# Performance work log

Hardware: AMD Instinct MI355X
Metric: run time of the kernel (lower is better)

## Reference

```python
import jax, jax.numpy as jnp
import numpy as np

HEADS = 6
FILTERS = (16, 32, 64)
V_FEATS = 11
N_NODES = 30000
N_EDGES = 480000


def setup_inputs() -> dict:
    key = jax.random.key(0)
    ks = jax.random.split(key, 20)
    d = {}
    d["x_int"] = jax.random.normal(ks[0], (N_NODES, V_FEATS), jnp.float32)
    d["x_nh"] = jax.random.normal(ks[1], (N_NODES, V_FEATS), jnp.float32)
    d["ei_int"] = jax.random.randint(ks[2], (2, N_EDGES), 0, N_NODES, jnp.int32)
    d["ei_nh"] = jax.random.randint(ks[3], (2, N_EDGES), 0, N_NODES, jnp.int32)
    f_in = V_FEATS
    kidx = 4
    for i, f in enumerate(FILTERS, 1):
        s = 1.0 / np.sqrt(f_in)
        d[f"W{i}"] = (jax.random.normal(ks[kidx], (f_in, HEADS * f), jnp.float32) * s); kidx += 1
        sa = 1.0 / np.sqrt(f)
        d[f"a{i}s"] = (jax.random.normal(ks[kidx], (HEADS, f), jnp.float32) * sa); kidx += 1
        d[f"a{i}d"] = (jax.random.normal(ks[kidx], (HEADS, f), jnp.float32) * sa); kidx += 1
        f_in = HEADS * f
    d["Wd"] = jax.random.normal(ks[kidx], (2 * HEADS * FILTERS[-1], 1), jnp.float32) * 0.05
    d["bd"] = jnp.zeros((1,), jnp.float32)
    return d


def _gat_layer(h, src, dst, W, a_s, a_d):
    """One multi-head graph-attention (DGAT) layer, heads concatenated.
    h: [N, F_in]; W: [F_in, H*F_out]; a_s, a_d: [H, F_out]."""
    N = h.shape[0]
    H, Fo = a_s.shape
    z = (h @ W).reshape(N, H, Fo)                      # [N, H, Fo]
    e_src = jnp.einsum('nhf,hf->nh', z, a_s)           # [N, H]
    e_dst = jnp.einsum('nhf,hf->nh', z, a_d)
    e = jax.nn.leaky_relu(e_src[src] + e_dst[dst], 0.2)  # [E, H]
    # softmax over incoming edges of each destination node
    e_max = jax.ops.segment_max(e, dst, num_segments=N)  # [N, H] (-inf for empty)
    ex = jnp.exp(e - e_max[dst])
    denom = jax.ops.segment_sum(ex, dst, num_segments=N)
    alpha = ex / (denom[dst] + 1e-16)                   # [E, H]
    msg = z[src] * alpha[:, :, None]                    # [E, H, Fo]
    out = jax.ops.segment_sum(msg, dst, num_segments=N) # [N, H, Fo]
    return jax.nn.elu(out).reshape(N, H * Fo)


def reference(x_int, x_nh, W1, a1s, a1d, W2, a2s, a2d, W3, a3s, a3d, Wd, bd, ei_int, ei_nh):
    layers = [(W1, a1s, a1d), (W2, a2s, a2d), (W3, a3s, a3d)]

    def run(h, ei):
        src, dst = ei[0], ei[1]
        for (W, a_s, a_d) in layers:
            h = _gat_layer(h, src, dst, W, a_s, a_d)
        return h

    hi = run(x_int, ei_int)   # [N, 384]
    hn = run(x_nh, ei_nh)     # [N, 384]
    x = jnp.concatenate([hi, hn], axis=1)       # [N, 768]
    x = jnp.sum(x, axis=0).reshape(1, -1)       # [1, 768] sum pooling
    norm = jnp.maximum(jnp.linalg.norm(x, axis=1, keepdims=True), 1e-12)
    x = x / norm                                # F.normalize
    x = x @ Wd + bd                             # Dense, linear nonlin
    return jnp.squeeze(x, 1)                    # [1]
```

## Files before the change

kernel.cpp:

```cpp
#include <hip/hip_runtime.h>
#include <math.h>

#define N_NODES 30000
#define N_EDGES 480000
#define HEADS   6
#define NN2 (2 * N_NODES)
#define NE2 (2 * N_EDGES)

typedef __attribute__((ext_vector_type(8))) short bf16x8;
typedef __attribute__((ext_vector_type(4))) float f32x4;
typedef __attribute__((ext_vector_type(2))) float f32x2;

__device__ __forceinline__ unsigned short f2bf(float f) {
    unsigned u = __float_as_uint(f);
    u += 0x7fffu + ((u >> 16) & 1u);
    return (unsigned short)(u >> 16);
}

__global__ void gemm1_es_kernel(const float* __restrict__ x0, const float* __restrict__ x1,
                                const float* __restrict__ W, const float* __restrict__ a_s,
                                const float* __restrict__ a_d,
                                unsigned char* __restrict__ zf8b, float* __restrict__ es8,
                                float* __restrict__ ed8) {
    constexpr int K = 11, HF = 96, TM = 16, Fo = 16;
    __shared__ float hs[TM * K];
    const int m0 = blockIdx.x * TM;
    const float* h = (m0 < N_NODES) ? (x0 + (size_t)m0 * K)
                                    : (x1 + (size_t)(m0 - N_NODES) * K);
    const int j = blockIdx.y * 64 + threadIdx.x;
    for (int idx = threadIdx.x; idx < TM * K; idx += 64) hs[idx] = h[idx];
    __syncthreads();
    if (j >= HF) return;
    float acc[TM];
#pragma unroll
    for (int m = 0; m < TM; ++m) acc[m] = 0.f;
    for (int k = 0; k < K; ++k) {
        float w = W[k * HF + j];
#pragma unroll
        for (int m = 0; m < TM; ++m) acc[m] = fmaf(hs[m * K + k], w, acc[m]);
    }
    const float as_v = a_s[j];
    const float ad_v = a_d[j];
    const int hh = j >> 4;
    const int fo = j & 15;
#pragma unroll
    for (int m = 0; m < TM; ++m) {
        const int pk = __builtin_amdgcn_cvt_pk_fp8_f32(acc[m], acc[m], 0, false);
        zf8b[((size_t)hh * NN2 + (m0 + m)) * Fo + fo] = (unsigned char)pk;
    }
#pragma unroll
    for (int m = 0; m < TM; ++m) {
        float ep = acc[m] * as_v;
        float dp = acc[m] * ad_v;
#pragma unroll
        for (int d = 1; d < 16; d <<= 1) {
            ep += __shfl_xor(ep, d);
            dp += __shfl_xor(dp, d);
        }
        if ((threadIdx.x & 15) == 0) {
            es8[(size_t)(m0 + m) * 8 + hh] = ep;
            ed8[(size_t)(m0 + m) * 8 + hh] = dp;
        }
    }
}

__global__ void convert_wt_kernel(const float* __restrict__ W, unsigned short* __restrict__ Wt,
                                  int K, int HF) {
    const int idx = blockIdx.x * 256 + threadIdx.x;
    if (idx >= K * HF) return;
    const int k = idx / HF;
    const int n = idx - k * HF;
    Wt[n * K + k] = f2bf(W[idx]);
}

template <int K, int HF>
__global__ __launch_bounds__(256) void gemm_es_kernel(
        const unsigned short* __restrict__ hbf, const unsigned short* __restrict__ Wt,
        const float* __restrict__ a_s, const float* __restrict__ a_d,
        unsigned char* __restrict__ zf8b, float* __restrict__ es8,
        float* __restrict__ ed8) {
    constexpr int KSTEPS = K / 32;
    constexpr int Fo  = HF / HEADS;
    constexpr int TPH = Fo / 16;
    const int wid = blockIdx.x * 4 + (threadIdx.x >> 6);
    if (wid >= NN2 / 16) return;
    const int lane = threadIdx.x & 63;
    const int r16  = lane & 15;
    const int quad = lane >> 4;
    const int m0 = wid * 16;

    bf16x8 afrag[KSTEPS];
    const unsigned short* ap = hbf + (size_t)(m0 + r16) * K + quad * 8;
#pragma unroll
    for (int i = 0; i < KSTEPS; ++i) afrag[i] = *(const bf16x8*)(ap + i * 32);

    const unsigned short* bp = Wt + (size_t)r16 * K + quad * 8;
    float es_p[4] = {0.f, 0.f, 0.f, 0.f};
    float ed_p[4] = {0.f, 0.f, 0.f, 0.f};
    for (int t = 0; t < HF / 16; ++t) {
        f32x4 acc = {0.f, 0.f, 0.f, 0.f};
        const unsigned short* bpt = bp + (size_t)t * 16 * K;
#pragma unroll
        for (int i = 0; i < KSTEPS; ++i) {
            const bf16x8 bfrag = *(const bf16x8*)(bpt + i * 32);
            acc = __builtin_amdgcn_mfma_f32_16x16x32_bf16(afrag[i], bfrag, acc, 0, 0, 0);
        }
        const float as_v = a_s[t * 16 + r16];
        const float ad_v = a_d[t * 16 + r16];
        const int th = t / TPH;
        const int fo = (t % TPH) * 16 + r16;
        unsigned char* zp = zf8b + ((size_t)th * NN2 + (m0 + quad * 4)) * Fo + fo;
#pragma unroll
        for (int r = 0; r < 4; ++r) {
            const int pk = __builtin_amdgcn_cvt_pk_fp8_f32(acc[r], acc[r], 0, false);
            zp[(size_t)r * Fo] = (unsigned char)pk;
            es_p[r] = fmaf(acc[r], as_v, es_p[r]);
            ed_p[r] = fmaf(acc[r], ad_v, ed_p[r]);
        }
        if (((t + 1) % TPH) == 0) {
            const int h = t / TPH;
#pragma unroll
            for (int r = 0; r < 4; ++r) {
                float ep = es_p[r], dp = ed_p[r];
#pragma unroll
                for (int d = 1; d < 16; d <<= 1) {
                    ep += __shfl_xor(ep, d);
                    dp += __shfl_xor(dp, d);
                }
                if (r16 == 0) {
                    es8[(size_t)(m0 + quad * 4 + r) * 8 + h] = ep;
                    ed8[(size_t)(m0 + quad * 4 + r) * 8 + h] = dp;
                }
                es_p[r] = 0.f;
                ed_p[r] = 0.f;
            }
        }
    }
}

__global__ void zero_int_kernel(int* __restrict__ p, int n) {
    const int i = blockIdx.x * 256 + threadIdx.x;
    if (i < n) p[i] = 0;
}

__global__ void hist2_kernel(const int* __restrict__ ei0, const int* __restrict__ ei1,
                             int* __restrict__ cnt) {
    const int e = blockIdx.x * 256 + threadIdx.x;
    if (e >= NE2) return;
    const int g = e >= N_EDGES;
    const int* ei = g ? ei1 : ei0;
    const int e2 = e - g * N_EDGES;
    atomicAdd(&cnt[g * N_NODES + ei[N_EDGES + e2]], 1);
}

#define SCAN_NB ((NN2 + 1023) / 1024)
__global__ void scan1_kernel(int* tmp, int* __restrict__ bsum) {
    __shared__ int s[1024];
    const int t = threadIdx.x;
    const int gid = blockIdx.x * 1024 + t;
    const int v = (gid < NN2) ? tmp[gid] : 0;
    s[t] = v;
    __syncthreads();
    for (int d = 1; d < 1024; d <<= 1) {
        int x = (t >= d) ? s[t - d] : 0;
        __syncthreads();
        s[t] += x;
        __syncthreads();
    }
    tmp[gid] = s[t] - v;
    if (t == 1023) bsum[blockIdx.x] = s[1023];
}

__global__ void scan2_kernel(int* __restrict__ bsum, int* __restrict__ boff) {
    if (threadIdx.x == 0) {
        int a = 0;
        for (int i = 0; i < SCAN_NB; ++i) { boff[i] = a; a += bsum[i]; }
        boff[SCAN_NB] = a;
    }
}

__global__ void scan3_kernel(int* tmp, const int* __restrict__ boff,
                             int* __restrict__ off) {
    const int gid = blockIdx.x * 1024 + threadIdx.x;
    if (gid < NN2) {
        const int o = tmp[gid] + boff[gid >> 10];
        off[gid] = o;
        tmp[gid] = o;
    }
    if (gid == 0) off[NN2] = boff[SCAN_NB];
}

__global__ void scatter2_kernel(const int* __restrict__ ei0, const int* __restrict__ ei1,
                                int* __restrict__ cursor,
                                unsigned short* __restrict__ csr16,
                                unsigned short* __restrict__ dst16) {
    const int e = blockIdx.x * 256 + threadIdx.x;
    if (e >= NE2) return;
    const int g = e >= N_EDGES;
    const int* ei = g ? ei1 : ei0;
    const int e2 = e - g * N_EDGES;
    const int src = g * N_NODES + ei[e2];
    const int dst = g * N_NODES + ei[N_EDGES + e2];
    const int slot = atomicAdd(&cursor[dst], 1);
    csr16[slot] = (unsigned short)src;
    dst16[slot] = (unsigned short)dst;
}

__global__ __launch_bounds__(256) void edgew_kernel(
        const unsigned short* __restrict__ csr16, const unsigned short* __restrict__ dst16,
        const float* __restrict__ es8, const float* __restrict__ ed8,
        unsigned* __restrict__ pA, unsigned* __restrict__ pB) {
    const int s = blockIdx.x * 256 + threadIdx.x;
    if (s >= NE2) return;
    const unsigned src = csr16[s];
    const unsigned dst = dst16[s];
    const f32x4 ea = *(const f32x4*)(es8 + src * 8u);
    const f32x2 eb = *(const f32x2*)(es8 + src * 8u + 4);
    const f32x4 da = *(const f32x4*)(ed8 + dst * 8u);
    const f32x2 db = *(const f32x2*)(ed8 + dst * 8u + 4);
    float ev[6];
    ev[0] = ea.x + da.x; ev[1] = ea.y + da.y; ev[2] = ea.z + da.z;
    ev[3] = ea.w + da.w; ev[4] = eb.x + db.x; ev[5] = eb.y + db.y;
#pragma unroll
    for (int h = 0; h < 6; ++h) {
        float v = ev[h];
        v = fmaxf(v, 0.2f * v);
        const unsigned rec = ((unsigned)f2bf(__expf(v)) << 16) | src;
        unsigned* p = (h < 3) ? (pA + (size_t)h * NE2) : (pB + (size_t)(h - 3) * NE2);
        p[s] = rec;
    }
}

template <int HF, int GS, int MAIN, int G>
__global__ __launch_bounds__(256) void agg_sub_kernel(
        const int* __restrict__ off, const unsigned* __restrict__ ewA,
        const unsigned* __restrict__ ewB,
        const unsigned* __restrict__ zf8, unsigned short* __restrict__ outz) {
    constexpr int Fo  = HF / HEADS;
    constexpr int L   = Fo / 4;
    constexpr int EPI = GS / L;
    constexpr int GPW = 64 / GS;
    constexpr int NB  = 4 * GPW;
    constexpr int BPH = NN2 / NB;
    int h, blk;
    {
        const int r = blockIdx.x & 7, g = blockIdx.x >> 3;
        if (r < 6) {
            if (g >= MAIN) return;
            h = r; blk = g;
        } else {
            const int k = (r - 6) * G + g;
            if (k >= 6 * (BPH - MAIN)) return;
            h = k % 6; blk = MAIN + k / 6;
        }
    }
    const int wavid = threadIdx.x >> 6;
    const int lane  = threadIdx.x & 63;
    const int grp = lane / GS;
    const int lg  = lane - grp * GS;
    const int eo = lg / L;
    const int fp = lg - eo * L;
    const int n = blk * NB + wavid * GPW + grp;

    const int s0  = off[n];
    const int deg = off[n + 1] - s0;
    const unsigned* ewp = ((h < 3) ? (ewA + (size_t)h * NE2)
                                   : (ewB + (size_t)(h - 3) * NE2)) + s0;
    const unsigned* zh = zf8 + (size_t)h * ((size_t)NN2 * L);

    float a0 = 0.f, a1 = 0.f, a2 = 0.f, a3 = 0.f, lsum = 0.f;
    for (int ib = 0; ib < deg; ib += 4 * EPI) {
        unsigned rec[4];
#pragma unroll
        for (int k = 0; k < 4; ++k) {
            const int idx = ib + k * EPI + eo;
            rec[k] = ewp[idx < deg ? idx : 0];
        }
        unsigned zz[4];
#pragma unroll
        for (int k = 0; k < 4; ++k)
            zz[k] = zh[(rec[k] & 0xFFFFu) * (unsigned)L + (unsigned)fp];
#pragma unroll
        for (int k = 0; k < 4; ++k) {
            const int idx = ib + k * EPI + eo;
            float ww = __uint_as_float(rec[k] & 0xFFFF0000u);
            ww = (idx < deg) ? ww : 0.f;
            lsum += ww;
            const f32x2 lo = __builtin_amdgcn_cvt_pk_f32_fp8((int)zz[k], false);
            const f32x2 hi = __builtin_amdgcn_cvt_pk_f32_fp8((int)zz[k], true);
            a0 = fmaf(ww, lo.x, a0);
            a1 = fmaf(ww, lo.y, a1);
            a2 = fmaf(ww, hi.x, a2);
            a3 = fmaf(ww, hi.y, a3);
        }
    }
#pragma unroll
    for (int d = L; d < GS; d <<= 1) {
        a0 += __shfl_xor(a0, d);
        a1 += __shfl_xor(a1, d);
        a2 += __shfl_xor(a2, d);
        a3 += __shfl_xor(a3, d);
        lsum += __shfl_xor(lsum, d);
    }
    if (eo == 0) {
        const float inv = 1.f / (lsum + 1e-16f);
        float o0 = a0 * inv, o1 = a1 * inv, o2 = a2 * inv, o3 = a3 * inv;
        o0 = o0 > 0.f ? o0 : (__expf(o0) - 1.f);
        o1 = o1 > 0.f ? o1 : (__expf(o1) - 1.f);
        o2 = o2 > 0.f ? o2 : (__expf(o2) - 1.f);
        o3 = o3 > 0.f ? o3 : (__expf(o3) - 1.f);
        unsigned short* op = outz + (size_t)n * HF + h * Fo + 4 * fp;
        *(unsigned*)op       = (unsigned)f2bf(o0) | ((unsigned)f2bf(o1) << 16);
        *(unsigned*)(op + 2) = (unsigned)f2bf(o2) | ((unsigned)f2bf(o3) << 16);
    }
}

#define POOL_BLOCKS 3072
#define POOL_WPH 2048
__global__ __launch_bounds__(256) void agg_pool_kernel(
        const int* __restrict__ off, const unsigned* __restrict__ ewA,
        const unsigned* __restrict__ ewB,
        const unsigned* __restrict__ zf8, float* __restrict__ pooled) {
    constexpr int Fo = 64, L = 16, EPI = 4;
    __shared__ float lds[128];
    int h, slot;
    {
        const int r = blockIdx.x & 7, g = blockIdx.x >> 3;
        if (r < 6) { h = r; slot = g; }
        else { h = g % 6; slot = 384 + (r - 6) * 64 + g / 6; }
    }
    const int wavid = threadIdx.x >> 6;
    const int ws    = slot * 4 + wavid;
    const int lane  = threadIdx.x & 63;
    const int eo = lane / L;
    const int fp = lane - eo * L;
    const unsigned* ewh = (h < 3) ? (ewA + (size_t)h * NE2)
                                  : (ewB + (size_t)(h - 3) * NE2);
    const unsigned* zh = zf8 + (size_t)h * ((size_t)NN2 * 16);

    if (threadIdx.x < 128) lds[threadIdx.x] = 0.f;
    __syncthreads();

    float p0[4] = {0.f, 0.f, 0.f, 0.f};
    float p1[4] = {0.f, 0.f, 0.f, 0.f};
    for (int n0 = 2 * ws; n0 < NN2; n0 += 2 * POOL_WPH) {
        const int oA = off[n0];
        const int oM = off[n0 + 1];
        const int oB = off[n0 + 2];
        const int degA = oM - oA, degB = oB - oM;
        const unsigned* eA = ewh + oA;
        const unsigned* eB = ewh + oM;
        float aA0 = 0.f, aA1 = 0.f, aA2 = 0.f, aA3 = 0.f, lsA = 0.f;
        float aB0 = 0.f, aB1 = 0.f, aB2 = 0.f, aB3 = 0.f, lsB = 0.f;
        const int dmax = degA > degB ? degA : degB;
        for (int ib = 0; ib < dmax; ib += 4 * EPI) {
            unsigned rA[4], rB[4];
#pragma unroll
            for (int k = 0; k < 4; ++k) {
                const int idx = ib + k * EPI + eo;
                rA[k] = eA[idx < degA ? idx : 0];
                rB[k] = eB[idx < degB ? idx : 0];
            }
            unsigned zA[4], zB[4];
#pragma unroll
            for (int k = 0; k < 4; ++k) {
                zA[k] = zh[(rA[k] & 0xFFFFu) * 16u + (unsigned)fp];
                zB[k] = zh[(rB[k] & 0xFFFFu) * 16u + (unsigned)fp];
            }
#pragma unroll
            for (int k = 0; k < 4; ++k) {
                const int idx = ib + k * EPI + eo;
                float wA = __uint_as_float(rA[k] & 0xFFFF0000u);
                float wB = __uint_as_float(rB[k] & 0xFFFF0000u);
                wA = (idx < degA) ? wA : 0.f;
                wB = (idx < degB) ? wB : 0.f;
                lsA += wA;
                lsB += wB;
                const f32x2 lA = __builtin_amdgcn_cvt_pk_f32_fp8((int)zA[k], false);
                const f32x2 hA = __builtin_amdgcn_cvt_pk_f32_fp8((int)zA[k], true);
                const f32x2 lB = __builtin_amdgcn_cvt_pk_f32_fp8((int)zB[k], false);
                const f32x2 hB = __builtin_amdgcn_cvt_pk_f32_fp8((int)zB[k], true);
                aA0 = fmaf(wA, lA.x, aA0);
                aA1 = fmaf(wA, lA.y, aA1);
                aA2 = fmaf(wA, hA.x, aA2);
                aA3 = fmaf(wA, hA.y, aA3);
                aB0 = fmaf(wB, lB.x, aB0);
                aB1 = fmaf(wB, lB.y, aB1);
                aB2 = fmaf(wB, hB.x, aB2);
                aB3 = fmaf(wB, hB.y, aB3);
            }
        }
#pragma unroll
        for (int d = L; d < 64; d <<= 1) {
            aA0 += __shfl_xor(aA0, d);
            aA1 += __shfl_xor(aA1, d);
            aA2 += __shfl_xor(aA2, d);
            aA3 += __shfl_xor(aA3, d);
            lsA += __shfl_xor(lsA, d);
            aB0 += __shfl_xor(aB0, d);
            aB1 += __shfl_xor(aB1, d);
            aB2 += __shfl_xor(aB2, d);
            aB3 += __shfl_xor(aB3, d);
            lsB += __shfl_xor(lsB, d);
        }
        if (eo == 0) {
            const float invA = 1.f / (lsA + 1e-16f);
            const float invB = 1.f / (lsB + 1e-16f);
            float oA0 = aA0 * invA, oA1 = aA1 * invA, oA2 = aA2 * invA, oA3 = aA3 * invA;
            float oB0 = aB0 * invB, oB1 = aB1 * invB, oB2 = aB2 * invB, oB3 = aB3 * invB;
            oA0 = oA0 > 0.f ? oA0 : (__expf(oA0) - 1.f);
            oA1 = oA1 > 0.f ? oA1 : (__expf(oA1) - 1.f);
            oA2 = oA2 > 0.f ? oA2 : (__expf(oA2) - 1.f);
            oA3 = oA3 > 0.f ? oA3 : (__expf(oA3) - 1.f);
            oB0 = oB0 > 0.f ? oB0 : (__expf(oB0) - 1.f);
            oB1 = oB1 > 0.f ? oB1 : (__expf(oB1) - 1.f);
            oB2 = oB2 > 0.f ? oB2 : (__expf(oB2) - 1.f);
            oB3 = oB3 > 0.f ? oB3 : (__expf(oB3) - 1.f);
            float* pp = (n0 < N_NODES) ? p0 : p1;
            pp[0] += oA0 + oB0;
            pp[1] += oA1 + oB1;
            pp[2] += oA2 + oB2;
            pp[3] += oA3 + oB3;
        }
    }
    if (eo == 0) {
#pragma unroll
        for (int j = 0; j < 4; ++j) {
            atomicAdd(&lds[4 * fp + j], p0[j]);
            atomicAdd(&lds[64 + 4 * fp + j], p1[j]);
        }
    }
    __syncthreads();
    if (threadIdx.x < 128) {
        const int g2 = threadIdx.x >> 6;
        const int f  = threadIdx.x & 63;
        atomicAdd(&pooled[g2 * 384 + h * Fo + f], lds[threadIdx.x]);
    }
}

__global__ void zero_pooled_kernel(float* __restrict__ p) {
    const int i = blockIdx.x * 256 + threadIdx.x;
    if (i < 768) p[i] = 0.f;
}

__global__ void final_kernel(const float* __restrict__ pooled, const float* __restrict__ Wd,
                             const float* __restrict__ bd, float* __restrict__ outp) {
    __shared__ float s_ss[256], s_dot[256];
    const int t = threadIdx.x;
    float ss = 0.f, dot = 0.f;
    for (int c = t; c < 768; c += 256) {
        const float v = pooled[c];
        ss  = fmaf(v, v, ss);
        dot = fmaf(v, Wd[c], dot);
    }
    s_ss[t] = ss; s_dot[t] = dot;
    __syncthreads();
    for (int off = 128; off > 0; off >>= 1) {
        if (t < off) { s_ss[t] += s_ss[t + off]; s_dot[t] += s_dot[t + off]; }
        __syncthreads();
    }
    if (t == 0) {
        const float norm = fmaxf(sqrtf(s_ss[0]), 1e-12f);
        outp[0] = s_dot[0] / norm + bd[0];
    }
}

extern "C" void kernel_launch(void* const* d_in, const int* in_sizes, int n_in,
                              void* d_out, int out_size, void* d_ws, size_t ws_size,
                              hipStream_t stream) {
    const float* x_int = (const float*)d_in[0];
    const float* x_nh  = (const float*)d_in[1];
    const int*   ei_int = (const int*)d_in[2];
    const int*   ei_nh  = (const int*)d_in[3];
    const float* W1  = (const float*)d_in[4];
    const float* a1s = (const float*)d_in[5];
    const float* a1d = (const float*)d_in[6];
    const float* W2  = (const float*)d_in[7];
    const float* a2s = (const float*)d_in[8];
    const float* a2d = (const float*)d_in[9];
    const float* W3  = (const float*)d_in[10];
    const float* a3s = (const float*)d_in[11];
    const float* a3d = (const float*)d_in[12];
    const float* Wd  = (const float*)d_in[13];
    const float* bd  = (const float*)d_in[14];
    float* out = (float*)d_out;

    unsigned short* hbf_a = (unsigned short*)d_ws;
    unsigned short* hbf_b = hbf_a + (size_t)NN2 * 96;
    unsigned short* wt2   = hbf_b + (size_t)NN2 * 192;
    unsigned short* wt3   = wt2   + (size_t)96 * 192;
    unsigned* zf8 = (unsigned*)(wt3 + (size_t)192 * 384);
    float* es8   = (float*)(zf8 + (size_t)NN2 * 96);
    float* ed8   = es8 + (size_t)NN2 * 8;
    float* pooled = ed8 + (size_t)NN2 * 8;
    int* tmp     = (int*)(pooled + 768);
    int* bsum    = tmp + SCAN_NB * 1024;
    int* boff    = bsum + SCAN_NB;
    int* off     = boff + SCAN_NB + 1;
    unsigned short* csr16 = (unsigned short*)(off + NN2 + 1);
    unsigned short* dst16 = csr16 + NE2;
    unsigned char* zf8b = (unsigned char*)zf8;

    unsigned* ew13A = (unsigned*)hbf_b;
    unsigned* ew13B = ew13A + (size_t)3 * NE2;
    unsigned* ew2A  = (unsigned*)hbf_a;
    unsigned* ew2B  = zf8 + (size_t)NN2 * 48;

    zero_pooled_kernel<<<3, 256, 0, stream>>>(pooled);
    convert_wt_kernel<<<(96 * 192 + 255) / 256, 256, 0, stream>>>(W2, wt2, 96, 192);
    convert_wt_kernel<<<(192 * 384 + 255) / 256, 256, 0, stream>>>(W3, wt3, 192, 384);

    zero_int_kernel<<<(NN2 + 255) / 256, 256, 0, stream>>>(tmp, NN2);
    hist2_kernel<<<(NE2 + 255) / 256, 256, 0, stream>>>(ei_int, ei_nh, tmp);
    scan1_kernel<<<SCAN_NB, 1024, 0, stream>>>(tmp, bsum);
    scan2_kernel<<<1, 64, 0, stream>>>(bsum, boff);
    scan3_kernel<<<SCAN_NB, 1024, 0, stream>>>(tmp, boff, off);
    scatter2_kernel<<<(NE2 + 255) / 256, 256, 0, stream>>>(ei_int, ei_nh, tmp, csr16, dst16);

    const int mfma_blocks = (NN2 / 16 + 3) / 4;
    const int ew_blocks = (NE2 + 255) / 256;

    gemm1_es_kernel<<<dim3(NN2 / 16, 2), 64, 0, stream>>>(x_int, x_nh, W1, a1s, a1d, zf8b,
                                                          es8, ed8);
    edgew_kernel<<<ew_blocks, 256, 0, stream>>>(csr16, dst16, es8, ed8, ew13A, ew13B);
    agg_sub_kernel<96, 16, 2812, 2814><<<8 * 2814, 256, 0, stream>>>(off, ew13A, ew13B,
                                                                     zf8, hbf_a);
    gemm_es_kernel<96, 192><<<mfma_blocks, 256, 0, stream>>>(hbf_a, wt2, a2s, a2d, zf8b,
                                                             es8, ed8);
    edgew_kernel<<<ew_blocks, 256, 0, stream>>>(csr16, dst16, es8, ed8, ew2A, ew2B);
    agg_sub_kernel<192, 32, 5625, 5625><<<45000, 256, 0, stream>>>(off, ew2A, ew2B,
                                                                   zf8, hbf_b);
    gemm_es_kernel<192, 384><<<mfma_blocks, 256, 0, stream>>>(hbf_b, wt3, a3s, a3d, zf8b,
                                                              es8, ed8);
    edgew_kernel<<<ew_blocks, 256, 0, stream>>>(csr16, dst16, es8, ed8, ew13A, ew13B);
    agg_pool_kernel<<<POOL_BLOCKS, 256, 0, stream>>>(off, ew13A, ew13B, zf8, pooled);

    final_kernel<<<1, 256, 0, stream>>>(pooled, Wd, bd, out);
}
```

Measured before the change: 577.9 us.

## Remap pooled aggregation to 4 lanes per node with 16-byte gathers

Reorganizes the final-layer aggregate-and-pool kernel so each wave handles 16 destination nodes, with four lanes per node each loading a 16-byte fp8 feature chunk and keeping 16 accumulators. This replaces the previous two-nodes-per-wave layout and removes its per-node cross-lane reductions, aiming for wider memory transactions and fewer shuffles. The cost is load imbalance, since each group loops to the maximum degree among its 16 nodes, plus higher register pressure.

```diff
diff --git a/kernel.cpp b/kernel.cpp
--- a/kernel.cpp
+++ b/kernel.cpp
@@ -10,6 +10,7 @@
 typedef __attribute__((ext_vector_type(8))) short bf16x8;
 typedef __attribute__((ext_vector_type(4))) float f32x4;
 typedef __attribute__((ext_vector_type(2))) float f32x2;
+typedef __attribute__((ext_vector_type(4))) unsigned u32x4;
 
 __device__ __forceinline__ unsigned short f2bf(float f) {
     unsigned u = __float_as_uint(f);
@@ -316,12 +317,11 @@
 }
 
 #define POOL_BLOCKS 3072
-#define POOL_WPH 2048
+#define POOL_WAVES 2048
 __global__ __launch_bounds__(256) void agg_pool_kernel(
         const int* __restrict__ off, const unsigned* __restrict__ ewA,
         const unsigned* __restrict__ ewB,
         const unsigned* __restrict__ zf8, float* __restrict__ pooled) {
-    constexpr int Fo = 64, L = 16, EPI = 4;
     __shared__ float lds[128];
     int h, slot;
     {
@@ -332,109 +332,101 @@
     const int wavid = threadIdx.x >> 6;
     const int ws    = slot * 4 + wavid;
     const int lane  = threadIdx.x & 63;
-    const int eo = lane / L;
-    const int fp = lane - eo * L;
+    const int c  = lane >> 2;
+    const int fp = lane & 3;
     const unsigned* ewh = (h < 3) ? (ewA + (size_t)h * NE2)
                                   : (ewB + (size_t)(h - 3) * NE2);
-    const unsigned* zh = zf8 + (size_t)h * ((size_t)NN2 * 16);
+    const u32x4* zq = (const u32x4*)(zf8 + (size_t)h * ((size_t)NN2 * 16));
 
     if (threadIdx.x < 128) lds[threadIdx.x] = 0.f;
     __syncthreads();
 
-    float p0[4] = {0.f, 0.f, 0.f, 0.f};
-    float p1[4] = {0.f, 0.f, 0.f, 0.f};
-    for (int n0 = 2 * ws; n0 < NN2; n0 += 2 * POOL_WPH) {
-        const int oA = off[n0];
-        const int oM = off[n0 + 1];
-        const int oB = off[n0 + 2];
-        const int degA = oM - oA, degB = oB - oM;
-        const unsigned* eA = ewh + oA;
-        const unsigned* eB = ewh + oM;
-        float aA0 = 0.f, aA1 = 0.f, aA2 = 0.f, aA3 = 0.f, lsA = 0.f;
-        float aB0 = 0.f, aB1 = 0.f, aB2 = 0.f, aB3 = 0.f, lsB = 0.f;
-        const int dmax = degA > degB ? degA : degB;
-        for (int ib = 0; ib < dmax; ib += 4 * EPI) {
-            unsigned rA[4], rB[4];
+    float p0[16], p1[16];
+#pragma unroll
+    for (int j = 0; j < 16; ++j) { p0[j] = 0.f; p1[j] = 0.f; }
+
+    for (int base = ws * 16; base < NN2; base += POOL_WAVES * 16) {
+        const int n = base + c;
+        const bool valid = n < NN2;
+        int s0 = 0, deg = 0;
+        if (valid) { s0 = off[n]; deg = off[n + 1] - s0; }
+        int dmx = deg;
+#pragma unroll
+        for (int d = 4; d < 64; d <<= 1) {
+            const int o = __shfl_xor(dmx, d);
+            dmx = o > dmx ? o : dmx;
+        }
+        const unsigned* ewp = ewh + s0;
+        float acc[16];
+#pragma unroll
+        for (int j = 0; j < 16; ++j) acc[j] = 0.f;
+        float lsum = 0.f;
+        for (int ib = 0; ib < dmx; ib += 4) {
+            unsigned rec[4];
 #pragma unroll
             for (int k = 0; k < 4; ++k) {
-                const int idx = ib + k * EPI + eo;
-                rA[k] = eA[idx < degA ? idx : 0];
-                rB[k] = eB[idx < degB ? idx : 0];
+                const int idx = ib + k;
+                rec[k] = ewp[idx < deg ? idx : 0];
             }
-            unsigned zA[4], zB[4];
+            u32x4 zz[4];
+#pragma unroll
+            for (int k = 0; k < 4; ++k)
+                zz[k] = zq[(rec[k] & 0xFFFFu) * 4u + (unsigned)fp];
 #pragma unroll
             for (int k = 0; k < 4; ++k) {
-                zA[k] = zh[(rA[k] & 0xFFFFu) * 16u + (unsigned)fp];
-                zB[k] = zh[(rB[k] & 0xFFFFu) * 16u + (unsigned)fp];
+                float w = __uint_as_float(rec[k] & 0xFFFF0000u);
+                w = ((ib + k) < deg) ? w : 0.f;
+                lsum += w;
+#pragma unroll
+                for (int d = 0; d < 4; ++d) {
+                    const f32x2 lo = __builtin_amdgcn_cvt_pk_f32_fp8((int)zz[k][d], false);
+                    const f32x2 hi = __builtin_amdgcn_cvt_pk_f32_fp8((int)zz[k][d], true);
+                    acc[4 * d + 0] = fmaf(w, lo.x, acc[4 * d + 0]);
+                    acc[4 * d + 1] = fmaf(w, lo.y, acc[4 * d + 1]);
+                    acc[4 * d + 2] = fmaf(w, hi.x, acc[4 * d + 2]);
+                    acc[4 * d + 3] = fmaf(w, hi.y, acc[4 * d + 3]);
+                }
             }
-#pragma unroll
-            for (int k = 0; k < 4; ++k) {
-                const int idx = ib + k * EPI + eo;
-                float wA = __uint_as_float(rA[k] & 0xFFFF0000u);
-                float wB = __uint_as_float(rB[k] & 0xFFFF0000u);
-                wA = (idx < degA) ? wA : 0.f;
-                wB = (idx < degB) ? wB : 0.f;
-                lsA += wA;
-                lsB += wB;
-                const f32x2 lA = __builtin_amdgcn_cvt_pk_f32_fp8((int)zA[k], false);
-                const f32x2 hA = __builtin_amdgcn_cvt_pk_f32_fp8((int)zA[k], true);
-                const f32x2 lB = __builtin_amdgcn_cvt_pk_f32_fp8((int)zB[k], false);
-                const f32x2 hB = __builtin_amdgcn_cvt_pk_f32_fp8((int)zB[k], true);
-                aA0 = fmaf(wA, lA.x, aA0);
-                aA1 = fmaf(wA, lA.y, aA1);
-                aA2 = fmaf(wA, hA.x, aA2);
-                aA3 = fmaf(wA, hA.y, aA3);
-                aB0 = fmaf(wB, lB.x, aB0);
-                aB1 = fmaf(wB, lB.y, aB1);
-                aB2 = fmaf(wB, hB.x, aB2);
-                aB3 = fmaf(wB, hB.y, aB3);
+        }
+        if (valid) {
+            const float inv = 1.f / (lsum + 1e-16f);
+            if (base < N_NODES) {
+#pragma unroll
+                for (int j = 0; j < 16; ++j) {
+                    float o = acc[j] * inv;
+                    o = o > 0.f ? o : (__expf(o) - 1.f);
+                    p0[j] += o;
+                }
+            } else {
+#pragma unroll
+                for (int j = 0; j < 16; ++j) {
+                    float o = acc[j] * inv;
+                    o = o > 0.f ? o : (__expf(o) - 1.f);
+                    p1[j] += o;
+                }
             }
         }
-#pragma unroll
-        for (int d = L; d < 64; d <<= 1) {
-            aA0 += __shfl_xor(aA0, d);
-            aA1 += __shfl_xor(aA1, d);
-            aA2 += __shfl_xor(aA2, d);
-            aA3 += __shfl_xor(aA3, d);
-            lsA += __shfl_xor(lsA, d);
-            aB0 += __shfl_xor(aB0, d);
-            aB1 += __shfl_xor(aB1, d);
-            aB2 += __shfl_xor(aB2, d);
-            aB3 += __shfl_xor(aB3, d);
-            lsB += __shfl_xor(lsB, d);
-        }
-        if (eo == 0) {
-            const float invA = 1.f / (lsA + 1e-16f);
-            const float invB = 1.f / (lsB + 1e-16f);
-            float oA0 = aA0 * invA, oA1 = aA1 * invA, oA2 = aA2 * invA, oA3 = aA3 * invA;
-            float oB0 = aB0 * invB, oB1 = aB1 * invB, oB2 = aB2 * invB, oB3 = aB3 * invB;
-            oA0 = oA0 > 0.f ? oA0 : (__expf(oA0) - 1.f);
-            oA1 = oA1 > 0.f ? oA1 : (__expf(oA1) - 1.f);
-            oA2 = oA2 > 0.f ? oA2 : (__expf(oA2) - 1.f);
-            oA3 = oA3 > 0.f ? oA3 : (__expf(oA3) - 1.f);
-            oB0 = oB0 > 0.f ? oB0 : (__expf(oB0) - 1.f);
-            oB1 = oB1 > 0.f ? oB1 : (__expf(oB1) - 1.f);
-            oB2 = oB2 > 0.f ? oB2 : (__expf(oB2) - 1.f);
-            oB3 = oB3 > 0.f ? oB3 : (__expf(oB3) - 1.f);
-            float* pp = (n0 < N_NODES) ? p0 : p1;
-            pp[0] += oA0 + oB0;
-            pp[1] += oA1 + oB1;
-            pp[2] += oA2 + oB2;
-            pp[3] += oA3 + oB3;
-        }
-    }
-    if (eo == 0) {
-#pragma unroll
-        for (int j = 0; j < 4; ++j) {
-            atomicAdd(&lds[4 * fp + j], p0[j]);
-            atomicAdd(&lds[64 + 4 * fp + j], p1[j]);
+    }
+#pragma unroll
+    for (int d = 4; d < 64; d <<= 1) {
+#pragma unroll
+        for (int j = 0; j < 16; ++j) {
+            p0[j] += __shfl_xor(p0[j], d);
+            p1[j] += __shfl_xor(p1[j], d);
+        }
+    }
+    if (lane < 4) {
+#pragma unroll
+        for (int j = 0; j < 16; ++j) {
+            atomicAdd(&lds[fp * 16 + j], p0[j]);
+            atomicAdd(&lds[64 + fp * 16 + j], p1[j]);
         }
     }
     __syncthreads();
     if (threadIdx.x < 128) {
         const int g2 = threadIdx.x >> 6;
         const int f  = threadIdx.x & 63;
-        atomicAdd(&pooled[g2 * 384 + h * Fo + f], lds[threadIdx.x]);
+        atomicAdd(&pooled[g2 * 384 + h * 64 + f], lds[threadIdx.x]);
     }
 }
 
```

Result: faster. 548.8 us (-5.0%).
